# Kernel optimization log

Measured on AMD Instinct MI355X. Metric: run time of the kernel, lower is better.

Reference implementation:

```python
import jax, jax.numpy as jnp
import numpy as np

NEG_SLOPE = 0.2


def gat_conv(x, W, att_s, att_d, bias, src, dst, heads, out_c, concat):
    n = x.shape[0]
    h = (x @ W).reshape(n, heads, out_c)                      # [N,H,C]
    a_s = (h * att_s).sum(-1)                                 # [N,H]
    a_d = (h * att_d).sum(-1)                                 # [N,H]
    logits = jax.nn.leaky_relu(a_s[src] + a_d[dst], NEG_SLOPE)  # [E,H]
    # segment softmax over incoming edges of each dst node (per head)
    m = jax.ops.segment_max(logits, dst, num_segments=n)
    e = jnp.exp(logits - m[dst])
    denom = jax.ops.segment_sum(e, dst, num_segments=n)
    alpha = e / denom[dst]                                    # [E,H]
    msg = h[src] * alpha[:, :, None]                          # [E,H,C]
    out = jax.ops.segment_sum(msg, dst, num_segments=n)       # [N,H,C]
    out = out.reshape(n, heads * out_c) if concat else out.mean(axis=1)
    return out + bias


def setup_inputs() -> dict:
    key = jax.random.key(0)
    ks = jax.random.split(key, 9)
    N, IN, OUT, E = 100000, 256, 40, 1600000
    return {
        "x": jax.random.normal(ks[0], (N, IN), jnp.float32),
        "edge_index": jax.random.randint(ks[1], (2, E), 0, N, jnp.int32),
        "W1": jax.random.normal(ks[2], (IN, 64), jnp.float32) * (1.0 / np.sqrt(IN)),
        "att_src1": jax.random.normal(ks[3], (8, 8), jnp.float32) * 0.1,
        "att_dst1": jax.random.normal(ks[4], (8, 8), jnp.float32) * 0.1,
        "b1": jnp.zeros((64,), jnp.float32),
        "W2": jax.random.normal(ks[5], (64, OUT), jnp.float32) * (1.0 / 8.0),
        "att_src2": jax.random.normal(ks[6], (1, OUT), jnp.float32) * 0.1,
        "att_dst2": jax.random.normal(ks[7], (1, OUT), jnp.float32) * 0.1,
        "b2": jnp.zeros((OUT,), jnp.float32),
    }


def reference(x, edge_index, W1, att_src1, att_dst1, b1, W2, att_src2, att_dst2, b2):
    n = x.shape[0]
    loop = jnp.arange(n, dtype=edge_index.dtype)
    src = jnp.concatenate([edge_index[0], loop])  # self-loops (PyG default)
    dst = jnp.concatenate([edge_index[1], loop])
    h = gat_conv(x, W1, att_src1, att_dst1, b1, src, dst, heads=8, out_c=8, concat=True)
    h = jax.nn.relu(h)
    out = gat_conv(h, W2, att_src2, att_dst2, b2, src, dst, heads=1, out_c=W2.shape[1], concat=True)
    return jax.nn.log_softmax(out, axis=1)
```

## Files before the change

kernel.cpp:

```cpp
#include <hip/hip_runtime.h>


#define L_IN   256
#define L_C1   64
#define L_H1   8
#define L_OUT  40
#define BCAP   5120

typedef __attribute__((ext_vector_type(8))) short short8;
typedef __attribute__((ext_vector_type(4))) float f32x4;

__device__ __forceinline__ float leaky(float x){ return fmaxf(x, 0.2f*x); }
__device__ __forceinline__ unsigned f2bf(float f){
  unsigned u = __float_as_uint(f);
  return (u + 0x7fffu + ((u >> 16) & 1u)) >> 16;
}
__device__ __forceinline__ float bflo(unsigned u){ return __uint_as_float(u << 16); }
__device__ __forceinline__ float bfhi(unsigned u){ return __uint_as_float(u & 0xffff0000u); }

__global__ __launch_bounds__(256) void prep_w1(const float* __restrict__ W1,
                                               ushort* __restrict__ wt,
                                               int* __restrict__ gcur, int NB){
  const int t = threadIdx.x;
  if (blockIdx.x == 4){
    for (int i = t; i < NB; i += 256) gcur[i] = 0;
    return;
  }
  __shared__ float ws[64][65];
  const int kb = blockIdx.x;
  #pragma unroll
  for (int i = 0; i < 16; ++i){
    int idx = t + i*256;
    ws[idx >> 6][idx & 63] = W1[(size_t)(kb*64 + (idx >> 6))*64 + (idx & 63)];
  }
  __syncthreads();
  int c  = t >> 2;
  int j0 = (t & 3) * 16;
  ushort tmp[16];
  #pragma unroll
  for (int j = 0; j < 16; ++j) tmp[j] = (ushort)f2bf(ws[j0 + j][c]);
  uint4* dst = (uint4*)(wt + (size_t)c*256 + kb*64 + j0);
  dst[0] = *(uint4*)&tmp[0];
  dst[1] = *(uint4*)&tmp[8];
}

__global__ __launch_bounds__(256) void bin_scatter(const int* __restrict__ esrc,
    const int* __restrict__ edst, int* __restrict__ gcur,
    unsigned* __restrict__ binned, int E, int NB){
  __shared__ int hist[512], rbase[512], cur[512];
  const int t  = threadIdx.x;
  const int e0 = blockIdx.x * 4096;
  hist[t] = 0; hist[t+256] = 0; cur[t] = 0; cur[t+256] = 0;
  __syncthreads();
  int sv[16], dv[16];
  const bool full = (e0 + 4096 <= E);
  if (full){
    #pragma unroll
    for (int j = 0; j < 4; ++j){
      int p4 = (e0 >> 2) + j*256 + t;
      int4 s4 = ((const int4*)esrc)[p4];
      int4 d4 = ((const int4*)edst)[p4];
      sv[4*j+0]=s4.x; sv[4*j+1]=s4.y; sv[4*j+2]=s4.z; sv[4*j+3]=s4.w;
      dv[4*j+0]=d4.x; dv[4*j+1]=d4.y; dv[4*j+2]=d4.z; dv[4*j+3]=d4.w;
      atomicAdd(&hist[d4.x >> 8], 1); atomicAdd(&hist[d4.y >> 8], 1);
      atomicAdd(&hist[d4.z >> 8], 1); atomicAdd(&hist[d4.w >> 8], 1);
    }
  } else {
    #pragma unroll
    for (int j = 0; j < 16; ++j){
      int idx = e0 + j*256 + t;
      if (idx < E){
        sv[j] = esrc[idx]; dv[j] = edst[idx];
        atomicAdd(&hist[dv[j] >> 8], 1);
      } else dv[j] = -1;
    }
  }
  __syncthreads();
  if (hist[t])                   rbase[t]     = atomicAdd(&gcur[t],     hist[t]);
  if (t+256 < NB && hist[t+256]) rbase[t+256] = atomicAdd(&gcur[t+256], hist[t+256]);
  __syncthreads();
  #pragma unroll
  for (int j = 0; j < 16; ++j){
    if (dv[j] >= 0){
      int b = dv[j] >> 8;
      int off = rbase[b] + atomicAdd(&cur[b], 1);
      if (off < BCAP)
        binned[(size_t)b*BCAP + off] =
          (unsigned)sv[j] | ((unsigned)(dv[j] & 255) << 17);
    }
  }
}

__global__ __launch_bounds__(256) void gemm1_kernel(
    const float* __restrict__ x, const ushort* __restrict__ wt,
    const float* __restrict__ atts, const float* __restrict__ attd,
    ushort* __restrict__ h1b, float* __restrict__ as1, float* __restrict__ ad1, int n)
{
  __shared__ __align__(16) char smem[34816];
  ushort (*xs)[136] = (ushort(*)[136])(smem);
  ushort (*ws)[136] = (ushort(*)[136])(smem + 17408);
  ushort (*hs)[72]  = (ushort(*)[72]) (smem);
  const int t  = threadIdx.x;
  const int rb = blockIdx.x * 64;
  const int wv = t >> 6;
  const int ln = t & 63;
  const int fr = ln & 15;
  const int fq = ln >> 4;

  #pragma unroll
  for (int i = 0; i < 8; ++i){
    int idx = t + i*256;
    int row = idx >> 5, c4 = idx & 31;
    float4 v = make_float4(0.f,0.f,0.f,0.f);
    if (rb + row < n) v = *(const float4*)(x + (size_t)(rb+row)*L_IN + c4*4);
    uint2 p;
    p.x = f2bf(v.x) | (f2bf(v.y) << 16);
    p.y = f2bf(v.z) | (f2bf(v.w) << 16);
    *(uint2*)&xs[row][c4*4] = p;
  }
  #pragma unroll
  for (int i = 0; i < 4; ++i){
    int idx = t + i*256;
    int row = idx >> 4, c8 = idx & 15;
    *(uint4*)&ws[row][c8*8] = *(const uint4*)(wt + (size_t)row*256 + c8*8);
  }
  __syncthreads();

  float4 px[8]; uint4 pw[4];
  #pragma unroll
  for (int i = 0; i < 8; ++i){
    int idx = t + i*256;
    int row = idx >> 5, c4 = idx & 31;
    px[i] = make_float4(0.f,0.f,0.f,0.f);
    if (rb + row < n) px[i] = *(const float4*)(x + (size_t)(rb+row)*L_IN + 128 + c4*4);
  }
  #pragma unroll
  for (int i = 0; i < 4; ++i){
    int idx = t + i*256;
    int row = idx >> 4, c8 = idx & 15;
    pw[i] = *(const uint4*)(wt + (size_t)row*256 + 128 + c8*8);
  }

  f32x4 acc[4];
  #pragma unroll
  for (int cb = 0; cb < 4; ++cb) acc[cb] = (f32x4){0.f,0.f,0.f,0.f};

  #pragma unroll
  for (int ks = 0; ks < 4; ++ks){
    short8 a = *(const short8*)&xs[wv*16 + fr][ks*32 + fq*8];
    #pragma unroll
    for (int cb = 0; cb < 4; ++cb){
      short8 b = *(const short8*)&ws[cb*16 + fr][ks*32 + fq*8];
      acc[cb] = __builtin_amdgcn_mfma_f32_16x16x32_bf16(a, b, acc[cb], 0, 0, 0);
    }
  }
  __syncthreads();

  #pragma unroll
  for (int i = 0; i < 8; ++i){
    int idx = t + i*256;
    int row = idx >> 5, c4 = idx & 31;
    uint2 p;
    p.x = f2bf(px[i].x) | (f2bf(px[i].y) << 16);
    p.y = f2bf(px[i].z) | (f2bf(px[i].w) << 16);
    *(uint2*)&xs[row][c4*4] = p;
  }
  #pragma unroll
  for (int i = 0; i < 4; ++i){
    int idx = t + i*256;
    int row = idx >> 4, c8 = idx & 15;
    *(uint4*)&ws[row][c8*8] = pw[i];
  }
  __syncthreads();

  #pragma unroll
  for (int ks = 0; ks < 4; ++ks){
    short8 a = *(const short8*)&xs[wv*16 + fr][ks*32 + fq*8];
    #pragma unroll
    for (int cb = 0; cb < 4; ++cb){
      short8 b = *(const short8*)&ws[cb*16 + fr][ks*32 + fq*8];
      acc[cb] = __builtin_amdgcn_mfma_f32_16x16x32_bf16(a, b, acc[cb], 0, 0, 0);
    }
  }
  __syncthreads();

  #pragma unroll
  for (int cb = 0; cb < 4; ++cb)
    #pragma unroll
    for (int r = 0; r < 4; ++r)
      hs[wv*16 + fq*4 + r][cb*16 + fr] = (ushort)f2bf(acc[cb][r]);
  __syncthreads();
  #pragma unroll
  for (int p = 0; p < 2; ++p){
    int pid = t + p*256;
    int row = pid >> 3, hd = pid & 7;
    if (rb + row < n){
      uint4 u = *(const uint4*)&hs[row][hd*8];
      float v0=bflo(u.x), v1=bfhi(u.x), v2=bflo(u.y), v3=bfhi(u.y);
      float v4=bflo(u.z), v5=bfhi(u.z), v6=bflo(u.w), v7=bfhi(u.w);
      const float* sa = atts + hd*8;
      const float* da = attd + hd*8;
      float ds = v0*sa[0]+v1*sa[1]+v2*sa[2]+v3*sa[3]+v4*sa[4]+v5*sa[5]+v6*sa[6]+v7*sa[7];
      float dd = v0*da[0]+v1*da[1]+v2*da[2]+v3*da[3]+v4*da[4]+v5*da[5]+v6*da[6]+v7*da[7];
      as1[(size_t)(rb+row)*L_H1 + hd] = ds;
      ad1[(size_t)(rb+row)*L_H1 + hd] = dd;
    }
  }
  #pragma unroll
  for (int i = 0; i < 2; ++i){
    int idx = t + i*256;
    int row = idx >> 3, c8 = idx & 7;
    if (rb + row < n)
      *(uint4*)(h1b + (size_t)(rb+row)*L_C1 + c8*8) = *(const uint4*)&hs[row][c8*8];
  }
}

__global__ __launch_bounds__(512) void bucket_csr(const unsigned* __restrict__ binned,
    const int* __restrict__ gcur, int2* __restrict__ nodeptr, int* __restrict__ csr,
    int N){
  __shared__ unsigned ebuf[BCAP];
  __shared__ int cnt[256], pref[256], cur[256];
  const int t = threadIdx.x;
  const int b = blockIdx.x;
  int ne = gcur[b]; if (ne > BCAP) ne = BCAP;
  const int base = b * BCAP;
  if (t < 256){ cnt[t] = 0; cur[t] = 0; }
  __syncthreads();
  for (int i = t; i < ne; i += 512){
    unsigned e = binned[base + i];
    ebuf[i] = e;
    atomicAdd(&cnt[(e >> 17) & 255u], 1);
  }
  __syncthreads();
  if (t < 256) pref[t] = cnt[t];
  __syncthreads();
  for (int off = 1; off < 256; off <<= 1){
    int a = 0;
    if (t < 256 && t >= off) a = pref[t-off];
    __syncthreads();
    if (t < 256) pref[t] += a;
    __syncthreads();
  }
  int excl = 0;
  if (t < 256) excl = pref[t] - cnt[t];
  __syncthreads();
  if (t < 256){
    pref[t] = excl;
    int d = (b << 8) + t;
    if (d < N) nodeptr[d] = make_int2(base + excl, cnt[t]);
  }
  __syncthreads();
  for (int i = t; i < ne; i += 512){
    unsigned e = ebuf[i];
    int ln = (int)((e >> 17) & 255u);
    int pos = base + pref[ln] + atomicAdd(&cur[ln], 1);
    csr[pos] = (int)(e & 0x1FFFFu);
  }
}

__global__ __launch_bounds__(256) void agg1_kernel(
    const int2* __restrict__ nodeptr, const int* __restrict__ csr,
    const ushort* __restrict__ h1b, const float* __restrict__ as1,
    const float* __restrict__ ad1, const float* __restrict__ b1,
    ushort* __restrict__ hrb, int n)
{
  int wid  = (blockIdx.x*blockDim.x + threadIdx.x) >> 6;
  int lane = threadIdx.x & 63;
  if (wid >= n) return;
  int2 np  = nodeptr[wid];
  int beg  = np.x;
  int degt = np.y + 1;

  const int h  = lane & 7;
  const int eg = lane >> 3;
  const int cp = lane & 31;
  const int ep = lane >> 5;
  const int hc = cp >> 2;

  float adn = ad1[(size_t)wid*L_H1 + h];
  float ax = 0.f, ay = 0.f, sp = 0.f;

  #define A1_GRP_W(g, SRCV, WV)                                            \
    { int i_ = (g)*8 + eg;                                                 \
      SRCV = (i_ < degt-1) ? csr[beg + i_] : wid;                          \
      float l_ = (i_ < degt) ? leaky(as1[(size_t)SRCV*L_H1 + h] + adn)     \
                             : -1e30f;                                     \
      WV = __expf(l_); sp += WV; }
  #define A1_GRP_G(SRCV, WV)                                               \
    _Pragma("unroll")                                                      \
    for (int e0 = 0; e0 < 8; e0 += 2){                                     \
      int e_  = e0 + ep;                                                   \
      float we_ = __shfl(WV,   e_*8 + hc);                                 \
      int   se_ = __shfl(SRCV, e_*8);                                      \
      unsigned u_ = *(const unsigned*)(h1b + (size_t)se_*L_C1 + cp*2);     \
      ax += we_ * bflo(u_);                                                \
      ay += we_ * bfhi(u_);                                                \
    }

  if (degt <= 16){
    int s0, s1; float w0, w1;
    A1_GRP_W(0, s0, w0) A1_GRP_W(1, s1, w1)
    A1_GRP_G(s0, w0) A1_GRP_G(s1, w1)
  } else if (degt <= 24){
    int s0, s1, s2; float w0, w1, w2;
    A1_GRP_W(0, s0, w0) A1_GRP_W(1, s1, w1) A1_GRP_W(2, s2, w2)
    A1_GRP_G(s0, w0) A1_GRP_G(s1, w1) A1_GRP_G(s2, w2)
  } else {
    const int ngrp = (degt + 7) >> 3;
    for (int g = 0; g < ngrp; ++g){
      int sg; float wg;
      A1_GRP_W(g, sg, wg)
      A1_GRP_G(sg, wg)
    }
  }
  #undef A1_GRP_W
  #undef A1_GRP_G

  #pragma unroll
  for (int off = 8; off < 64; off <<= 1) sp += __shfl_xor(sp, off);
  float rinv = 1.0f / __shfl(sp, hc);
  ax += __shfl_xor(ax, 32);
  ay += __shfl_xor(ay, 32);
  if (lane < 32){
    float2 bv = *(const float2*)&b1[cp*2];
    float r0 = fmaxf(ax*rinv + bv.x, 0.f);
    float r1 = fmaxf(ay*rinv + bv.y, 0.f);
    *(unsigned*)(hrb + (size_t)wid*L_C1 + cp*2) = f2bf(r0) | (f2bf(r1) << 16);
  }
}

__global__ __launch_bounds__(256) void gemm2_kernel(
    const ushort* __restrict__ hrb, const float* __restrict__ W2,
    const float* __restrict__ atts2, const float* __restrict__ attd2,
    ushort* __restrict__ h2b, float* __restrict__ as2, float* __restrict__ ad2, int n)
{
  __shared__ float w2s[64*40];
  const int t = threadIdx.x;
  for (int i = t; i < 64*40; i += 256) w2s[i] = W2[i];
  __syncthreads();
  int row = blockIdx.x*256 + t;
  if (row >= n) return;

  uint4 rv[8];
  #pragma unroll
  for (int q = 0; q < 8; ++q)
    rv[q] = *(const uint4*)(hrb + (size_t)row*L_C1 + q*8);

  f32x4 acc4[10];
  #pragma unroll
  for (int j = 0; j < 10; ++j) acc4[j] = (f32x4){0.f,0.f,0.f,0.f};

  #pragma unroll
  for (int q = 0; q < 8; ++q){
    unsigned uu[4] = {rv[q].x, rv[q].y, rv[q].z, rv[q].w};
    #pragma unroll
    for (int d = 0; d < 4; ++d){
      int k = q*8 + d*2;
      float v0 = bflo(uu[d]), v1 = bfhi(uu[d]);
      const f32x4* w0 = (const f32x4*)&w2s[k*40];
      const f32x4* w1 = (const f32x4*)&w2s[(k+1)*40];
      #pragma unroll
      for (int j = 0; j < 10; ++j) acc4[j] += v0*w0[j] + v1*w1[j];
    }
  }

  float acc[40];
  #pragma unroll
  for (int j = 0; j < 10; ++j){
    acc[4*j+0]=acc4[j][0]; acc[4*j+1]=acc4[j][1];
    acc[4*j+2]=acc4[j][2]; acc[4*j+3]=acc4[j][3];
  }
  float ps = 0.f, pd = 0.f;
  #pragma unroll
  for (int j = 0; j < 40; ++j){ ps += acc[j]*atts2[j]; pd += acc[j]*attd2[j]; }
  unsigned pk[20];
  #pragma unroll
  for (int q = 0; q < 20; ++q) pk[q] = f2bf(acc[2*q]) | (f2bf(acc[2*q+1]) << 16);
  uint4* dst = (uint4*)(h2b + (size_t)row*L_OUT);
  #pragma unroll
  for (int q = 0; q < 5; ++q) dst[q] = make_uint4(pk[4*q],pk[4*q+1],pk[4*q+2],pk[4*q+3]);
  as2[row] = ps;
  ad2[row] = pd;
}

__global__ __launch_bounds__(256) void agg2_kernel(
    const int2* __restrict__ nodeptr, const int* __restrict__ csr,
    const ushort* __restrict__ h2b, const float* __restrict__ as2,
    const float* __restrict__ ad2, const float* __restrict__ b2,
    float* __restrict__ out, int n)
{
  int wid  = (blockIdx.x*blockDim.x + threadIdx.x) >> 6;
  int lane = threadIdx.x & 63;
  if (wid >= n) return;
  int2 np  = nodeptr[wid];
  int beg  = np.x;
  int degt = np.y + 1;

  const int eidx = (lane < 60) ? (lane / 20) : 0;
  const int cq   = (lane < 60) ? (lane % 20) : 0;

  float adn = ad2[wid];
  float ax = 0.f, ay = 0.f, sp = 0.f;

  #define A2_STEP(e_, SRCV, WV, CNT)                                       \
    { int ee_ = (e_);                                                      \
      int es_ = (ee_ < 64) ? ee_ : 63;                                     \
      float we_ = __shfl(WV,   es_);                                       \
      int   se_ = __shfl(SRCV, es_);                                       \
      we_ = (ee_ < (CNT)) ? we_ : 0.f;                                     \
      unsigned u_ = *(const unsigned*)(h2b + (size_t)se_*L_OUT + cq*2);    \
      ax += we_ * bflo(u_);                                                \
      ay += we_ * bfhi(u_); }

  if (degt <= 64){
    int i = lane;
    int src = (i < degt-1) ? csr[beg + i] : wid;
    float l = (i < degt) ? leaky(as2[src] + adn) : -1e30f;
    float w = __expf(l);
    sp = w;
    if (degt <= 18){
      #pragma unroll
      for (int j = 0; j < 2; ++j){
        A2_STEP(j*9 + 0*3 + eidx, src, w, degt)
        A2_STEP(j*9 + 1*3 + eidx, src, w, degt)
        A2_STEP(j*9 + 2*3 + eidx, src, w, degt)
      }
    } else if (degt <= 27){
      #pragma unroll
      for (int j = 0; j < 3; ++j){
        A2_STEP(j*9 + 0*3 + eidx, src, w, degt)
        A2_STEP(j*9 + 1*3 + eidx, src, w, degt)
        A2_STEP(j*9 + 2*3 + eidx, src, w, degt)
      }
    } else if (degt <= 36){
      #pragma unroll
      for (int j = 0; j < 4; ++j){
        A2_STEP(j*9 + 0*3 + eidx, src, w, degt)
        A2_STEP(j*9 + 1*3 + eidx, src, w, degt)
        A2_STEP(j*9 + 2*3 + eidx, src, w, degt)
      }
    } else {
      for (int e0 = 0; e0 < degt; e0 += 9){
        A2_STEP(e0 + 0*3 + eidx, src, w, degt)
        A2_STEP(e0 + 1*3 + eidx, src, w, degt)
        A2_STEP(e0 + 2*3 + eidx, src, w, degt)
      }
    }
  } else {
    const int ngrp = (degt + 63) >> 6;
    for (int g = 0; g < ngrp; ++g){
      int i = g*64 + lane;
      int src = (i < degt-1) ? csr[beg + i] : wid;
      float l = (i < degt) ? leaky(as2[src] + adn) : -1e30f;
      float w = __expf(l);
      sp += w;
      int cnt = degt - g*64; if (cnt > 64) cnt = 64;
      for (int e0 = 0; e0 < cnt; e0 += 9){
        A2_STEP(e0 + 0*3 + eidx, src, w, cnt)
        A2_STEP(e0 + 1*3 + eidx, src, w, cnt)
        A2_STEP(e0 + 2*3 + eidx, src, w, cnt)
      }
    }
  }
  #undef A2_STEP

  #pragma unroll
  for (int off = 1; off < 64; off <<= 1) sp += __shfl_xor(sp, off);
  float rinv = 1.0f / sp;

  float ax0 = __shfl(ax, cq), ax1 = __shfl(ax, cq+20), ax2 = __shfl(ax, cq+40);
  float ay0 = __shfl(ay, cq), ay1 = __shfl(ay, cq+20), ay2 = __shfl(ay, cq+40);
  float axs = (ax0 + ax1) + ax2;
  float ays = (ay0 + ay1) + ay2;

  bool act = (lane < 20);
  float o0 = axs*rinv + b2[cq*2];
  float o1 = ays*rinv + b2[cq*2+1];
  float mx = act ? fmaxf(o0, o1) : -1e30f;
  #pragma unroll
  for (int off = 1; off < 32; off <<= 1) mx = fmaxf(mx, __shfl_xor(mx, off));
  float ex = act ? (__expf(o0 - mx) + __expf(o1 - mx)) : 0.f;
  #pragma unroll
  for (int off = 1; off < 32; off <<= 1) ex += __shfl_xor(ex, off);
  float lse = mx + __logf(ex);
  if (act){
    float2 r = make_float2(o0 - lse, o1 - lse);
    *(float2*)(out + (size_t)wid*L_OUT + cq*2) = r;
  }
}

extern "C" void kernel_launch(void* const* d_in, const int* in_sizes, int n_in,
                              void* d_out, int out_size, void* d_ws, size_t ws_size,
                              hipStream_t stream)
{
  const float* x    = (const float*)d_in[0];
  const int*   ei   = (const int*)  d_in[1];
  const float* W1   = (const float*)d_in[2];
  const float* as1w = (const float*)d_in[3];
  const float* ad1w = (const float*)d_in[4];
  const float* b1   = (const float*)d_in[5];
  const float* W2   = (const float*)d_in[6];
  const float* as2w = (const float*)d_in[7];
  const float* ad2w = (const float*)d_in[8];
  const float* b2   = (const float*)d_in[9];

  const int N = in_sizes[0] / L_IN;
  const int E = in_sizes[1] / 2;
  const int NB = (N + 255) >> 8;
  const int NSC = (E + 4095) / 4096;
  const int* esrc = ei;
  const int* edst = ei + E;
  float* out = (float*)d_out;

  char* w = (char*)d_ws;
  auto alloc = [&](size_t bytes)->char*{
    char* p = w; w += (bytes + 255) & ~size_t(255); return p;
  };
  ushort* h1b  = (ushort*)alloc((size_t)N*L_C1*2);
  float*  as1  = (float*) alloc((size_t)N*L_H1*4);
  float*  ad1  = (float*) alloc((size_t)N*L_H1*4);
  size_t union_sz = (size_t)N*L_C1*2 + (size_t)N*L_OUT*2;
  if (union_sz < (size_t)NB*BCAP*4) union_sz = (size_t)NB*BCAP*4;
  char*  ub    = alloc(union_sz);
  ushort* hrb  = (ushort*)ub;
  ushort* h2b  = (ushort*)(ub + (size_t)N*L_C1*2);
  unsigned* binned = (unsigned*)ub;
  float*  as2  = (float*) alloc((size_t)N*4);
  float*  ad2  = (float*) alloc((size_t)N*4);
  ushort* wt   = (ushort*)alloc((size_t)64*256*2);
  int2*  nodeptr=(int2*)  alloc((size_t)N*8);
  int*   csr   = (int*)   alloc((size_t)NB*BCAP*4);
  int*   gcur  = (int*)   alloc((size_t)NB*4);

  prep_w1     <<<5,          256, 0, stream>>>(W1, wt, gcur, NB);
  bin_scatter <<<NSC,        256, 0, stream>>>(esrc, edst, gcur, binned, E, NB);
  gemm1_kernel<<<(N+63)/64,  256, 0, stream>>>(x, wt, as1w, ad1w, h1b, as1, ad1, N);
  bucket_csr  <<<NB,         512, 0, stream>>>(binned, gcur, nodeptr, csr, N);
  agg1_kernel <<<(N+3)/4,    256, 0, stream>>>(nodeptr, csr, h1b, as1, ad1, b1, hrb, N);
  gemm2_kernel<<<(N+255)/256,256, 0, stream>>>(hrb, W2, as2w, ad2w, h2b, as2, ad2, N);
  agg2_kernel <<<(N+3)/4,    256, 0, stream>>>(nodeptr, csr, h2b, as2, ad2, b2, out, N);
}
```

Before: 185.5 us.

## Make gemm1 persistent with resident W tile and direct x-to-register MFMA operands

gemm1 becomes a persistent kernel of at most 768 blocks that keeps the full bf16 W1 tile (64x256) in shared memory and loops over 64-row tiles. Each wave now loads its x rows from global straight into registers, converts them to bf16 and feeds them to MFMA without staging through LDS. This removes most block-wide syncs and the repeated per-block W loads. The epilogue becomes per-wave, with each wave writing its own rows and computing the attention dots. The trade-off is less memory-level parallelism per block, and x loads are no longer coalesced through shared memory.

```diff
diff --git a/kernel.cpp b/kernel.cpp
--- a/kernel.cpp
+++ b/kernel.cpp
@@ -94,14 +94,12 @@
 __global__ __launch_bounds__(256) void gemm1_kernel(
     const float* __restrict__ x, const ushort* __restrict__ wt,
     const float* __restrict__ atts, const float* __restrict__ attd,
-    ushort* __restrict__ h1b, float* __restrict__ as1, float* __restrict__ ad1, int n)
+    ushort* __restrict__ h1b, float* __restrict__ as1, float* __restrict__ ad1,
+    int n, int ntiles, int npb)
 {
-  __shared__ __align__(16) char smem[34816];
-  ushort (*xs)[136] = (ushort(*)[136])(smem);
-  ushort (*ws)[136] = (ushort(*)[136])(smem + 17408);
-  ushort (*hs)[72]  = (ushort(*)[72]) (smem);
+  __shared__ ushort ws[64][264];
+  __shared__ ushort hs[64][72];
   const int t  = threadIdx.x;
-  const int rb = blockIdx.x * 64;
   const int wv = t >> 6;
   const int ln = t & 63;
   const int fr = ln & 15;
@@ -110,108 +108,67 @@
   #pragma unroll
   for (int i = 0; i < 8; ++i){
     int idx = t + i*256;
-    int row = idx >> 5, c4 = idx & 31;
-    float4 v = make_float4(0.f,0.f,0.f,0.f);
-    if (rb + row < n) v = *(const float4*)(x + (size_t)(rb+row)*L_IN + c4*4);
-    uint2 p;
-    p.x = f2bf(v.x) | (f2bf(v.y) << 16);
-    p.y = f2bf(v.z) | (f2bf(v.w) << 16);
-    *(uint2*)&xs[row][c4*4] = p;
-  }
-  #pragma unroll
-  for (int i = 0; i < 4; ++i){
-    int idx = t + i*256;
-    int row = idx >> 4, c8 = idx & 15;
+    int row = idx >> 5, c8 = idx & 31;
     *(uint4*)&ws[row][c8*8] = *(const uint4*)(wt + (size_t)row*256 + c8*8);
   }
   __syncthreads();
 
-  float4 px[8]; uint4 pw[4];
-  #pragma unroll
-  for (int i = 0; i < 8; ++i){
-    int idx = t + i*256;
-    int row = idx >> 5, c4 = idx & 31;
-    px[i] = make_float4(0.f,0.f,0.f,0.f);
-    if (rb + row < n) px[i] = *(const float4*)(x + (size_t)(rb+row)*L_IN + 128 + c4*4);
-  }
-  #pragma unroll
-  for (int i = 0; i < 4; ++i){
-    int idx = t + i*256;
-    int row = idx >> 4, c8 = idx & 15;
-    pw[i] = *(const uint4*)(wt + (size_t)row*256 + 128 + c8*8);
-  }
-
-  f32x4 acc[4];
-  #pragma unroll
-  for (int cb = 0; cb < 4; ++cb) acc[cb] = (f32x4){0.f,0.f,0.f,0.f};
-
-  #pragma unroll
-  for (int ks = 0; ks < 4; ++ks){
-    short8 a = *(const short8*)&xs[wv*16 + fr][ks*32 + fq*8];
-    #pragma unroll
-    for (int cb = 0; cb < 4; ++cb){
-      short8 b = *(const short8*)&ws[cb*16 + fr][ks*32 + fq*8];
-      acc[cb] = __builtin_amdgcn_mfma_f32_16x16x32_bf16(a, b, acc[cb], 0, 0, 0);
-    }
-  }
-  __syncthreads();
-
-  #pragma unroll
-  for (int i = 0; i < 8; ++i){
-    int idx = t + i*256;
-    int row = idx >> 5, c4 = idx & 31;
-    uint2 p;
-    p.x = f2bf(px[i].x) | (f2bf(px[i].y) << 16);
-    p.y = f2bf(px[i].z) | (f2bf(px[i].w) << 16);
-    *(uint2*)&xs[row][c4*4] = p;
-  }
-  #pragma unroll
-  for (int i = 0; i < 4; ++i){
-    int idx = t + i*256;
-    int row = idx >> 4, c8 = idx & 15;
-    *(uint4*)&ws[row][c8*8] = pw[i];
-  }
-  __syncthreads();
-
-  #pragma unroll
-  for (int ks = 0; ks < 4; ++ks){
-    short8 a = *(const short8*)&xs[wv*16 + fr][ks*32 + fq*8];
-    #pragma unroll
-    for (int cb = 0; cb < 4; ++cb){
-      short8 b = *(const short8*)&ws[cb*16 + fr][ks*32 + fq*8];
-      acc[cb] = __builtin_amdgcn_mfma_f32_16x16x32_bf16(a, b, acc[cb], 0, 0, 0);
-    }
-  }
-  __syncthreads();
-
-  #pragma unroll
-  for (int cb = 0; cb < 4; ++cb)
-    #pragma unroll
-    for (int r = 0; r < 4; ++r)
-      hs[wv*16 + fq*4 + r][cb*16 + fr] = (ushort)f2bf(acc[cb][r]);
-  __syncthreads();
-  #pragma unroll
-  for (int p = 0; p < 2; ++p){
-    int pid = t + p*256;
-    int row = pid >> 3, hd = pid & 7;
-    if (rb + row < n){
-      uint4 u = *(const uint4*)&hs[row][hd*8];
-      float v0=bflo(u.x), v1=bfhi(u.x), v2=bflo(u.y), v3=bfhi(u.y);
-      float v4=bflo(u.z), v5=bfhi(u.z), v6=bflo(u.w), v7=bfhi(u.w);
-      const float* sa = atts + hd*8;
-      const float* da = attd + hd*8;
-      float ds = v0*sa[0]+v1*sa[1]+v2*sa[2]+v3*sa[3]+v4*sa[4]+v5*sa[5]+v6*sa[6]+v7*sa[7];
-      float dd = v0*da[0]+v1*da[1]+v2*da[2]+v3*da[3]+v4*da[4]+v5*da[5]+v6*da[6]+v7*da[7];
-      as1[(size_t)(rb+row)*L_H1 + hd] = ds;
-      ad1[(size_t)(rb+row)*L_H1 + hd] = dd;
-    }
-  }
-  #pragma unroll
-  for (int i = 0; i < 2; ++i){
-    int idx = t + i*256;
-    int row = idx >> 3, c8 = idx & 7;
-    if (rb + row < n)
-      *(uint4*)(h1b + (size_t)(rb+row)*L_C1 + c8*8) = *(const uint4*)&hs[row][c8*8];
+  for (int tile = blockIdx.x; tile < ntiles; tile += npb){
+    const int rb = tile * 64;
+    const int ar = rb + wv*16 + fr;
+    const bool rv = ar < n;
+    const float* xr = x + (size_t)(rv ? ar : 0) * L_IN;
+
+    f32x4 acc[4];
+    #pragma unroll
+    for (int cb = 0; cb < 4; ++cb) acc[cb] = (f32x4){0.f,0.f,0.f,0.f};
+
+    #pragma unroll
+    for (int kk = 0; kk < 8; ++kk){
+      const int k0 = kk*32 + fq*8;
+      float4 a0 = make_float4(0.f,0.f,0.f,0.f), a1 = a0;
+      if (rv){
+        a0 = *(const float4*)(xr + k0);
+        a1 = *(const float4*)(xr + k0 + 4);
+      }
+      uint4 au;
+      au.x = f2bf(a0.x) | (f2bf(a0.y) << 16);
+      au.y = f2bf(a0.z) | (f2bf(a0.w) << 16);
+      au.z = f2bf(a1.x) | (f2bf(a1.y) << 16);
+      au.w = f2bf(a1.z) | (f2bf(a1.w) << 16);
+      short8 a = *(short8*)&au;
+      #pragma unroll
+      for (int cb = 0; cb < 4; ++cb){
+        short8 b = *(const short8*)&ws[cb*16 + fr][k0];
+        acc[cb] = __builtin_amdgcn_mfma_f32_16x16x32_bf16(a, b, acc[cb], 0, 0, 0);
+      }
+    }
+
+    #pragma unroll
+    for (int cb = 0; cb < 4; ++cb)
+      #pragma unroll
+      for (int r = 0; r < 4; ++r)
+        hs[wv*16 + fq*4 + r][cb*16 + fr] = (ushort)f2bf(acc[cb][r]);
+
+    #pragma unroll
+    for (int i = 0; i < 2; ++i){
+      int task = ln + i*64;
+      int lrow = task >> 3;
+      int sub  = task & 7;
+      int row  = rb + wv*16 + lrow;
+      if (row < n){
+        uint4 u = *(const uint4*)&hs[wv*16 + lrow][sub*8];
+        *(uint4*)(h1b + (size_t)row*L_C1 + sub*8) = u;
+        float v0=bflo(u.x), v1=bfhi(u.x), v2=bflo(u.y), v3=bfhi(u.y);
+        float v4=bflo(u.z), v5=bfhi(u.z), v6=bflo(u.w), v7=bfhi(u.w);
+        const float* sa = atts + sub*8;
+        const float* da = attd + sub*8;
+        float ds = v0*sa[0]+v1*sa[1]+v2*sa[2]+v3*sa[3]+v4*sa[4]+v5*sa[5]+v6*sa[6]+v7*sa[7];
+        float dd = v0*da[0]+v1*da[1]+v2*da[2]+v3*da[3]+v4*da[4]+v5*da[5]+v6*da[6]+v7*da[7];
+        as1[(size_t)row*L_H1 + sub] = ds;
+        ad1[(size_t)row*L_H1 + sub] = dd;
+      }
+    }
   }
 }
 
@@ -508,6 +465,8 @@
   const int E = in_sizes[1] / 2;
   const int NB = (N + 255) >> 8;
   const int NSC = (E + 4095) / 4096;
+  const int NT1 = (N + 63) / 64;
+  const int NPB = (NT1 < 768) ? NT1 : 768;
   const int* esrc = ei;
   const int* edst = ei + E;
   float* out = (float*)d_out;
@@ -534,7 +493,8 @@
 
   prep_w1     <<<5,          256, 0, stream>>>(W1, wt, gcur, NB);
   bin_scatter <<<NSC,        256, 0, stream>>>(esrc, edst, gcur, binned, E, NB);
-  gemm1_kernel<<<(N+63)/64,  256, 0, stream>>>(x, wt, as1w, ad1w, h1b, as1, ad1, N);
+  gemm1_kernel<<<NPB,        256, 0, stream>>>(x, wt, as1w, ad1w, h1b, as1, ad1,
+                                               N, NT1, NPB);
   bucket_csr  <<<NB,         512, 0, stream>>>(binned, gcur, nodeptr, csr, N);
   agg1_kernel <<<(N+3)/4,    256, 0, stream>>>(nodeptr, csr, h1b, as1, ad1, b1, hrb, N);
   gemm2_kernel<<<(N+255)/256,256, 0, stream>>>(hrb, W2, as2w, ad2w, h2b, as2, ad2, N);
```

New measurement: 183.8 us. No clear change (-0.9%).
